# Kernel tuning notes

Hardware: AMD Instinct MI355X
Metric: run time of the kernel (lower is better)

Reference implementation:

```python
import jax, jax.numpy as jnp
import numpy as np

N_HEADS = 16
ROPE_DIMS = 16
SEQ_LEN = 512


def _rope_cache(T, dtype=jnp.float32):
    rd = ROPE_DIMS
    freqs = 1.0 / (10000.0 ** (jnp.arange(0, rd, 2, dtype=jnp.float32) / rd))  # [rd/2]
    t = jnp.arange(T, dtype=jnp.float32)
    ang = jnp.outer(t, freqs)  # [T, rd/2]
    return jnp.cos(ang).astype(dtype), jnp.sin(ang).astype(dtype)


def _apply_rope(x, cos, sin):
    # x: [B, H, T, hd]; partial RoPE on first ROPE_DIMS dims
    rd = ROPE_DIMS
    x_rope, x_pass = x[..., :rd], x[..., rd:]
    x1, x2 = x_rope[..., : rd // 2], x_rope[..., rd // 2 :]
    # cos/sin: [T, rd/2] -> broadcast over B, H
    out = jnp.concatenate([x1 * cos - x2 * sin, x2 * cos + x1 * sin], axis=-1)
    return jnp.concatenate([out, x_pass], axis=-1)


def setup_inputs() -> dict:
    key = jax.random.key(0)
    k1, k2, k3 = jax.random.split(key, 3)
    B, T, C = 8, SEQ_LEN, 2048
    x = jax.random.normal(k1, (B, T, C), dtype=jnp.float32)
    Wqkv = jax.random.normal(k2, (3 * C, C), dtype=jnp.float32) * (1.0 / np.sqrt(C))
    Wout = jax.random.normal(k3, (C, C), dtype=jnp.float32) * (1.0 / np.sqrt(C))
    return {"x": x, "Wqkv": Wqkv, "Wout": Wout}


def reference(x, Wqkv, Wout):
    B, T, C = x.shape
    H = N_HEADS
    hd = C // H
    # fused QKV projection
    qkv = jnp.einsum("btc,fc->btf", x, Wqkv)  # [B, T, 3C]
    qkv = qkv.reshape(B, T, 3, H, hd)
    q, k, v = qkv[:, :, 0], qkv[:, :, 1], qkv[:, :, 2]  # [B, T, H, hd]
    q = jnp.transpose(q, (0, 2, 1, 3))  # [B, H, T, hd]
    k = jnp.transpose(k, (0, 2, 1, 3))
    v = jnp.transpose(v, (0, 2, 1, 3))
    cos, sin = _rope_cache(T, dtype=x.dtype)
    q = _apply_rope(q, cos, sin)
    k = _apply_rope(k, cos, sin)
    # causal SDPA
    scale = 1.0 / np.sqrt(hd)
    scores = jnp.einsum("bhqd,bhkd->bhqk", q, k) * scale
    causal = jnp.tril(jnp.ones((T, T), dtype=bool))
    scores = jnp.where(causal, scores, jnp.finfo(scores.dtype).min)
    attn = jax.nn.softmax(scores, axis=-1)
    y = jnp.einsum("bhqk,bhkd->bhqd", attn, v)  # [B, H, T, hd]
    y = jnp.transpose(y, (0, 2, 1, 3)).reshape(B, T, C)
    return jnp.einsum("btc,oc->bto", y, Wout)
```

## Files before the change

### kernel.cpp

```cpp
#include <hip/hip_runtime.h>

typedef __bf16 bf16_t;
typedef __bf16 bf16x4 __attribute__((ext_vector_type(4)));
typedef __bf16 bf16x8 __attribute__((ext_vector_type(8)));
typedef float f32x4 __attribute__((ext_vector_type(4)));

#define GLB(p) ((const __attribute__((address_space(1))) void*)(p))
#define LDS(p) ((__attribute__((address_space(3))) void*)(p))

__global__ void f32_to_bf16(const float* __restrict__ src, bf16_t* __restrict__ dst, int n8)
{
    const int i = blockIdx.x * 256 + threadIdx.x;
    if (i >= n8) return;
    const f32x4 a = *(const f32x4*)&src[(size_t)i * 8];
    const f32x4 b = *(const f32x4*)&src[(size_t)i * 8 + 4];
    bf16x8 h = {(bf16_t)a[0], (bf16_t)a[1], (bf16_t)a[2], (bf16_t)a[3],
                (bf16_t)b[0], (bf16_t)b[1], (bf16_t)b[2], (bf16_t)b[3]};
    *(bf16x8*)&dst[(size_t)i * 8] = h;
}

#define LDB4(d, kk, S)                                                         \
    { _Pragma("unroll") for (int nt = 0; nt < 4; ++nt)                         \
        bfr[S][nt] = *(const bf16x8*)&smem[sBe + (d) * 32768 + (kk) * 8192 + nt * 512]; }

#define LDA4(d, kk, g, S)                                                      \
    { _Pragma("unroll") for (int i = 0; i < 4; ++i)                            \
        afr[S][i] = *(const bf16x8*)&smem[sAe + (d) * 32768 + (kk) * 8192 + ((g) * 4 + i) * 512]; }

#define MM4(g, SA, SB)                                                         \
    { _Pragma("unroll") for (int i = 0; i < 4; ++i)                            \
        _Pragma("unroll") for (int nt = 0; nt < 4; ++nt)                       \
            acc[(g) * 4 + i][nt] = __builtin_amdgcn_mfma_f32_16x16x32_bf16(    \
                afr[SA][i], bfr[SB][nt], acc[(g) * 4 + i][nt], 0, 0, 0); }

#define PHASE_TAIL(g, SA, SB)                                                  \
    __builtin_amdgcn_s_barrier();                                              \
    asm volatile("s_waitcnt lgkmcnt(0)" ::: "memory");                         \
    __builtin_amdgcn_s_setprio(1);                                             \
    MM4(g, SA, SB);                                                            \
    __builtin_amdgcn_s_setprio(0);                                             \
    __builtin_amdgcn_s_barrier();

template <int MODE>
__global__ __launch_bounds__(512, 2)
void gemm256(const bf16_t* __restrict__ A, const bf16_t* __restrict__ Bm, int K,
             bf16_t* __restrict__ o0, bf16_t* __restrict__ o1, bf16_t* __restrict__ o2,
             float* __restrict__ of)
{
    __shared__ __align__(16) bf16_t smem[65536];

    const int tid  = threadIdx.x;
    const int lane = tid & 63;
    const int w    = tid >> 6;
    const int wr   = w >> 2;
    const int wc   = w & 3;
    const int quad = lane >> 4;
    const int qcol = lane & 15;
    const int m0   = blockIdx.x * 256;
    const int n0   = blockIdx.y * 256;

    f32x4 acc[8][4];
#pragma unroll
    for (int i = 0; i < 8; ++i)
#pragma unroll
        for (int j = 0; j < 4; ++j)
            acc[i][j] = (f32x4){0.f, 0.f, 0.f, 0.f};

    const int srow = w * 16 + (lane >> 2);
    const int scg  = (lane & 3) ^ ((lane >> 3) & 3);
    const bf16_t* Ag = A  + (size_t)(m0 + srow) * K + scg * 8;
    const bf16_t* Bg = Bm + (size_t)(n0 + srow) * K + scg * 8;

    auto STAGE = [&](int d, int t, int hh) {
        const int isA = hh & 1;
        const int kh  = hh >> 1;
        const bf16_t* g = (isA ? Ag : Bg) + t * 64 + kh * 32;
        bf16_t* l = &smem[d * 32768 + kh * 8192 + (isA ? 0 : 16384) + w * 512];
        __builtin_amdgcn_global_load_lds(GLB(g), LDS(l), 16, 0, 0);
        __builtin_amdgcn_global_load_lds(GLB(g + (size_t)128 * K), LDS(l + 4096), 16, 0, 0);
    };

    const int rs8 = (quad ^ ((qcol >> 1) & 3)) * 8;
    const int sAe = (wr * 128 + qcol) * 32 + rs8;
    const int sBe = 16384 + (wc * 64 + qcol) * 32 + rs8;

    bf16x8 afr[2][4], bfr[2][4];

    const int NT  = K >> 6;
    const int NIT = NT >> 1;

    STAGE(0, 0, 0); STAGE(0, 0, 1); STAGE(0, 0, 2); STAGE(0, 0, 3);
    STAGE(1, 1, 0); STAGE(1, 1, 1); STAGE(1, 1, 2);
    asm volatile("s_waitcnt vmcnt(6)" ::: "memory");
    __builtin_amdgcn_s_barrier();

    for (int J = 0; J < NIT - 1; ++J) {
        const int t = 2 * J;
        LDB4(0, 0, 0); LDA4(0, 0, 0, 0); STAGE(1, t + 1, 3);
        PHASE_TAIL(0, 0, 0);
        LDA4(0, 0, 1, 1); STAGE(0, t + 2, 0);
        PHASE_TAIL(1, 1, 0);
        LDB4(0, 1, 1); LDA4(0, 1, 0, 0); STAGE(0, t + 2, 1);
        PHASE_TAIL(0, 0, 1);
        LDA4(0, 1, 1, 1); STAGE(0, t + 2, 2);
        asm volatile("s_waitcnt vmcnt(6)" ::: "memory");
        PHASE_TAIL(1, 1, 1);
        LDB4(1, 0, 0); LDA4(1, 0, 0, 0); STAGE(0, t + 2, 3);
        PHASE_TAIL(0, 0, 0);
        LDA4(1, 0, 1, 1); STAGE(1, t + 3, 0);
        PHASE_TAIL(1, 1, 0);
        LDB4(1, 1, 1); LDA4(1, 1, 0, 0); STAGE(1, t + 3, 1);
        PHASE_TAIL(0, 0, 1);
        LDA4(1, 1, 1, 1); STAGE(1, t + 3, 2);
        asm volatile("s_waitcnt vmcnt(6)" ::: "memory");
        PHASE_TAIL(1, 1, 1);
    }

    {
        const int t = NT - 2;
        LDB4(0, 0, 0); LDA4(0, 0, 0, 0); STAGE(1, t + 1, 3);
        PHASE_TAIL(0, 0, 0);
        LDA4(0, 0, 1, 1);
        PHASE_TAIL(1, 1, 0);
        LDB4(0, 1, 1); LDA4(0, 1, 0, 0);
        PHASE_TAIL(0, 0, 1);
        LDA4(0, 1, 1, 1);
        asm volatile("s_waitcnt vmcnt(0)" ::: "memory");
        PHASE_TAIL(1, 1, 1);
        LDB4(1, 0, 0); LDA4(1, 0, 0, 0);
        PHASE_TAIL(0, 0, 0);
        LDA4(1, 0, 1, 1);
        PHASE_TAIL(1, 1, 0);
        LDB4(1, 1, 1); LDA4(1, 1, 0, 0);
        PHASE_TAIL(0, 0, 1);
        LDA4(1, 1, 1, 1);
        __builtin_amdgcn_s_barrier();
        asm volatile("s_waitcnt lgkmcnt(0)" ::: "memory");
        __builtin_amdgcn_s_setprio(1);
        MM4(1, 1, 1);
        __builtin_amdgcn_s_setprio(0);
    }

#pragma unroll
    for (int mt = 0; mt < 8; ++mt) {
#pragma unroll
        for (int nt = 0; nt < 4; ++nt) {
#pragma unroll
            for (int r = 0; r < 4; ++r) {
                const int m = m0 + wr * 128 + mt * 16 + quad * 4 + r;
                const int f = n0 + wc * 64 + nt * 16 + qcol;
                const float val = acc[mt][nt][r];
                if (MODE == 0) {
                    const int b     = m >> 9;
                    const int t     = m & 511;
                    const int which = f >> 11;
                    const int h     = (f >> 7) & 15;
                    const int d     = f & 127;
                    if (which == 2) {
                        o2[((size_t)(((b << 4) + h) * 128 + d) << 9) + t] = (bf16_t)val;
                    } else {
                        bf16_t* dst = (which == 0) ? o0 : o1;
                        dst[(size_t)(((b << 4) + h) * 512 + t) * 128 + d] = (bf16_t)val;
                    }
                } else {
                    of[(size_t)m * 2048 + f] = val;
                }
            }
        }
    }
}

template <int MODE>
__global__ __launch_bounds__(256)
void gemm_bt(const bf16_t* __restrict__ A, const bf16_t* __restrict__ Bm, int K,
             bf16_t* __restrict__ o0, bf16_t* __restrict__ o1, bf16_t* __restrict__ o2,
             float* __restrict__ of)
{
    __shared__ __align__(16) bf16_t As[128 * 32];
    __shared__ __align__(16) bf16_t Bs[128 * 32];
    const int tid  = threadIdx.x;
    const int lane = tid & 63;
    const int w    = tid >> 6;
    const int wm   = (w & 1) * 64;
    const int wn   = (w >> 1) * 64;
    const int m0   = blockIdx.x * 128;
    const int n0   = blockIdx.y * 128;
    const int quad = lane >> 4;
    const int qcol = lane & 15;

    f32x4 acc[4][4];
#pragma unroll
    for (int i = 0; i < 4; ++i)
#pragma unroll
        for (int j = 0; j < 4; ++j)
            acc[i][j] = (f32x4){0.f, 0.f, 0.f, 0.f};

    const int rc = lane >> 2;
    const int cg = (lane & 3) ^ (rc & 3);
    const int c0 = 2 * w, c1 = 2 * w + 1;
    const bf16_t* ag0 = A  + (size_t)(m0 + 16 * c0 + rc) * K + cg * 8;
    const bf16_t* ag1 = A  + (size_t)(m0 + 16 * c1 + rc) * K + cg * 8;
    const bf16_t* bg0 = Bm + (size_t)(n0 + 16 * c0 + rc) * K + cg * 8;
    const bf16_t* bg1 = Bm + (size_t)(n0 + 16 * c1 + rc) * K + cg * 8;
    bf16_t* al0 = &As[c0 * 512];
    bf16_t* al1 = &As[c1 * 512];
    bf16_t* bl0 = &Bs[c0 * 512];
    bf16_t* bl1 = &Bs[c1 * 512];

    const int swz8 = (quad ^ (qcol & 3)) * 8;

    for (int k0 = 0; k0 < K; k0 += 32) {
        __syncthreads();
        __builtin_amdgcn_global_load_lds(GLB(ag0 + k0), LDS(al0), 16, 0, 0);
        __builtin_amdgcn_global_load_lds(GLB(ag1 + k0), LDS(al1), 16, 0, 0);
        __builtin_amdgcn_global_load_lds(GLB(bg0 + k0), LDS(bl0), 16, 0, 0);
        __builtin_amdgcn_global_load_lds(GLB(bg1 + k0), LDS(bl1), 16, 0, 0);
        __syncthreads();

        bf16x8 af[4], bf[4];
#pragma unroll
        for (int mt = 0; mt < 4; ++mt)
            af[mt] = *(const bf16x8*)&As[(wm + mt * 16 + qcol) * 32 + swz8];
#pragma unroll
        for (int nt = 0; nt < 4; ++nt)
            bf[nt] = *(const bf16x8*)&Bs[(wn + nt * 16 + qcol) * 32 + swz8];
#pragma unroll
        for (int mt = 0; mt < 4; ++mt)
#pragma unroll
            for (int nt = 0; nt < 4; ++nt)
                acc[mt][nt] = __builtin_amdgcn_mfma_f32_16x16x32_bf16(af[mt], bf[nt], acc[mt][nt], 0, 0, 0);
    }

#pragma unroll
    for (int mt = 0; mt < 4; ++mt) {
#pragma unroll
        for (int nt = 0; nt < 4; ++nt) {
#pragma unroll
            for (int r = 0; r < 4; ++r) {
                const int m = m0 + wm + mt * 16 + quad * 4 + r;
                const int f = n0 + wn + nt * 16 + qcol;
                const float val = acc[mt][nt][r];
                of[(size_t)m * 2048 + f] = val;
            }
        }
    }
}

__global__ void rope_kernel(bf16_t* __restrict__ q, bf16_t* __restrict__ k)
{
    const int id  = blockIdx.x * 256 + threadIdx.x;
    const int arr = id >> 19;
    const int rem = id & ((1 << 19) - 1);
    const int bh  = rem >> 12;
    const int t   = (rem >> 3) & 511;
    const int d   = rem & 7;

    bf16_t* p = (arr ? k : q) + (size_t)(bh * 512 + t) * 128;
    const float x1 = (float)p[d];
    const float x2 = (float)p[d + 8];
    const float freq = __expf(-(float)d * 1.1512925464970229f);
    const float ang  = (float)t * freq;
    const float c = cosf(ang), s = sinf(ang);
    p[d]     = (bf16_t)(x1 * c - x2 * s);
    p[d + 8] = (bf16_t)(x2 * c + x1 * s);
}

#define PLD 72

__global__ __launch_bounds__(256)
void flash_attn(const bf16_t* __restrict__ q, const bf16_t* __restrict__ k,
                const bf16_t* __restrict__ vT, bf16_t* __restrict__ y)
{
    const int bid = blockIdx.x;
    const int sg  = bid >> 7;
    const int qtb = (sg < 2) ? sg : 5 - sg;
    const int rem = bid & 127;
    const int h   = rem & 15;
    const int b   = rem >> 4;
    const int tid  = threadIdx.x;
    const int lane = tid & 63;
    const int w    = tid >> 6;
    const int quad = lane >> 4;
    const int qcol = lane & 15;

    __shared__ __align__(16) bf16_t Ps[128 * PLD];

    const bf16_t* qb  = q  + (size_t)((b * 16 + h) * 512) * 128;
    const bf16_t* kb  = k  + (size_t)((b * 16 + h) * 512) * 128;
    const bf16_t* vtb = vT + (size_t)((b * 16 + h) * 128) * 512;

    bf16x8 qfrag[2][4];
#pragma unroll
    for (int qg = 0; qg < 2; ++qg) {
        const int qrow = qtb * 128 + w * 32 + qg * 16 + qcol;
#pragma unroll
        for (int kc = 0; kc < 4; ++kc)
            qfrag[qg][kc] = *(const bf16x8*)&qb[(size_t)qrow * 128 + kc * 32 + quad * 8];
    }

    f32x4 acc_o[2][8];
#pragma unroll
    for (int qg = 0; qg < 2; ++qg)
#pragma unroll
        for (int nt = 0; nt < 8; ++nt) acc_o[qg][nt] = (f32x4){0.f, 0.f, 0.f, 0.f};
    float m_run[2] = {-INFINITY, -INFINITY};
    float l_run[2] = {0.f, 0.f};
    const float scale = 0.08838834764831845f;

    const int wq_min  = qtb * 128 + w * 32;
    const int kt_last = 2 * qtb + 1;
    for (int kt = 0; kt <= kt_last; ++kt) {
        if (kt * 64 > wq_min + 31) break;
        const bool need_mask = ((kt + 1) * 64 > wq_min);

        f32x4 sacc[2][4];
#pragma unroll
        for (int qg = 0; qg < 2; ++qg)
#pragma unroll
            for (int mt = 0; mt < 4; ++mt) sacc[qg][mt] = (f32x4){0.f, 0.f, 0.f, 0.f};
#pragma unroll
        for (int mt = 0; mt < 4; ++mt)
#pragma unroll
            for (int kc = 0; kc < 4; ++kc) {
                bf16x8 af = *(const bf16x8*)&kb[(size_t)(kt * 64 + mt * 16 + qcol) * 128 + kc * 32 + quad * 8];
                sacc[0][mt] = __builtin_amdgcn_mfma_f32_16x16x32_bf16(af, qfrag[0][kc], sacc[0][mt], 0, 0, 0);
                sacc[1][mt] = __builtin_amdgcn_mfma_f32_16x16x32_bf16(af, qfrag[1][kc], sacc[1][mt], 0, 0, 0);
            }

#pragma unroll
        for (int qg = 0; qg < 2; ++qg) {
            float s[16];
#pragma unroll
            for (int mt = 0; mt < 4; ++mt)
#pragma unroll
                for (int r = 0; r < 4; ++r)
                    s[mt * 4 + r] = sacc[qg][mt][r] * scale;
            if (need_mask) {
                const int qglob = qtb * 128 + w * 32 + qg * 16 + qcol;
#pragma unroll
                for (int mt = 0; mt < 4; ++mt)
#pragma unroll
                    for (int r = 0; r < 4; ++r)
                        if (kt * 64 + mt * 16 + quad * 4 + r > qglob)
                            s[mt * 4 + r] = -1e30f;
            }

            float mx = s[0];
#pragma unroll
            for (int i = 1; i < 16; ++i) mx = fmaxf(mx, s[i]);
            mx = fmaxf(mx, __shfl_xor(mx, 16));
            mx = fmaxf(mx, __shfl_xor(mx, 32));
            const float m_new = fmaxf(m_run[qg], mx);
            const float alpha = __expf(m_run[qg] - m_new);
            float p16[16];
            float sum = 0.f;
#pragma unroll
            for (int i = 0; i < 16; ++i) { p16[i] = __expf(s[i] - m_new); sum += p16[i]; }
            sum += __shfl_xor(sum, 16);
            sum += __shfl_xor(sum, 32);
            l_run[qg] = l_run[qg] * alpha + sum;
            m_run[qg] = m_new;

#pragma unroll
            for (int mt = 0; mt < 4; ++mt) {
                bf16x4 pb = {(bf16_t)p16[mt * 4 + 0], (bf16_t)p16[mt * 4 + 1],
                             (bf16_t)p16[mt * 4 + 2], (bf16_t)p16[mt * 4 + 3]};
                *(bf16x4*)&Ps[(w * 32 + qg * 16 + qcol) * PLD + mt * 16 + quad * 4] = pb;
            }

#pragma unroll
            for (int r = 0; r < 4; ++r) {
                const float ar = __shfl(alpha, quad * 4 + r);
#pragma unroll
                for (int nt = 0; nt < 8; ++nt)
                    acc_o[qg][nt][r] *= ar;
            }
        }

#pragma unroll
        for (int kc2 = 0; kc2 < 2; ++kc2) {
            bf16x8 pf0 = *(const bf16x8*)&Ps[(w * 32 + qcol) * PLD + kc2 * 32 + quad * 8];
            bf16x8 pf1 = *(const bf16x8*)&Ps[(w * 32 + 16 + qcol) * PLD + kc2 * 32 + quad * 8];
#pragma unroll
            for (int nt = 0; nt < 8; ++nt) {
                bf16x8 vf = *(const bf16x8*)&vtb[(size_t)(nt * 16 + qcol) * 512 + kt * 64 + kc2 * 32 + quad * 8];
                acc_o[0][nt] = __builtin_amdgcn_mfma_f32_16x16x32_bf16(pf0, vf, acc_o[0][nt], 0, 0, 0);
                acc_o[1][nt] = __builtin_amdgcn_mfma_f32_16x16x32_bf16(pf1, vf, acc_o[1][nt], 0, 0, 0);
            }
        }
    }

#pragma unroll
    for (int qg = 0; qg < 2; ++qg) {
#pragma unroll
        for (int r = 0; r < 4; ++r) {
            const float lr = __shfl(l_run[qg], quad * 4 + r);
            const int t  = qtb * 128 + w * 32 + qg * 16 + quad * 4 + r;
#pragma unroll
            for (int nt = 0; nt < 8; ++nt) {
                const int cc = h * 128 + nt * 16 + qcol;
                y[(size_t)(b * 512 + t) * 2048 + cc] = (bf16_t)(acc_o[qg][nt][r] / lr);
            }
        }
    }
}

extern "C" void kernel_launch(void* const* d_in, const int* in_sizes, int n_in,
                              void* d_out, int out_size, void* d_ws, size_t ws_size,
                              hipStream_t stream)
{
    (void)in_sizes; (void)n_in; (void)out_size; (void)ws_size;

    const float* x    = (const float*)d_in[0];
    const float* Wqkv = (const float*)d_in[1];
    const float* Wout = (const float*)d_in[2];
    float* out = (float*)d_out;

    const size_t SEG = (size_t)8 * 16 * 512 * 128;
    bf16_t* q      = (bf16_t*)d_ws;
    bf16_t* k      = q + SEG;
    bf16_t* vT     = k + SEG;
    bf16_t* xb     = vT + SEG;
    bf16_t* y      = xb;
    bf16_t* Wqkvb  = xb + SEG;
    bf16_t* Woutb  = Wqkvb + (size_t)6144 * 2048;

    f32_to_bf16<<<(8388608 / 8) / 256, 256, 0, stream>>>(x, xb, 8388608 / 8);
    f32_to_bf16<<<(12582912 / 8) / 256, 256, 0, stream>>>(Wqkv, Wqkvb, 12582912 / 8);
    f32_to_bf16<<<(4194304 / 8) / 256, 256, 0, stream>>>(Wout, Woutb, 4194304 / 8);
    gemm256<0><<<dim3(4096 / 256, 6144 / 256), 512, 0, stream>>>(xb, Wqkvb, 2048, q, k, vT, nullptr);
    rope_kernel<<<(2 * 128 * 512 * 8) / 256, 256, 0, stream>>>(q, k);
    flash_attn<<<512, 256, 0, stream>>>(q, k, vT, y);
    gemm_bt<1><<<dim3(4096 / 128, 2048 / 128), 256, 0, stream>>>(y, Woutb, 2048, nullptr, nullptr, nullptr, out);
}
```

Before: 381.3 us.

## Stage K and V^T tiles in shared memory for flash attention

Each K and V^T tile is now loaded cooperatively into padded LDS buffers once per block, instead of every wave reading its fragments directly from global memory. This is meant to cut redundant global and L2 traffic, since all four waves share the same K/V tile. The score MFMA loop is also moved inside the per-qg loop to lower register pressure. In exchange it adds two barriers per key tile and LDS usage that may reduce occupancy. Waves past the causal boundary must keep looping to join the barriers, which adds idle iterations.

Result: no change. 377.7 us (-0.9%).

```diff
diff --git a/kernel.cpp b/kernel.cpp
--- a/kernel.cpp
+++ b/kernel.cpp
@@ -265,6 +265,8 @@
     p[d + 8] = (bf16_t)(x2 * c + x1 * s);
 }
 
+#define KLD 132
+#define VLD 68
 #define PLD 72
 
 __global__ __launch_bounds__(256)
@@ -283,6 +285,8 @@
     const int quad = lane >> 4;
     const int qcol = lane & 15;
 
+    __shared__ __align__(16) bf16_t Ks[64 * KLD];
+    __shared__ __align__(16) bf16_t VTs[128 * VLD];
     __shared__ __align__(16) bf16_t Ps[128 * PLD];
 
     const bf16_t* qb  = q  + (size_t)((b * 16 + h) * 512) * 128;
@@ -310,31 +314,41 @@
     const int wq_min  = qtb * 128 + w * 32;
     const int kt_last = 2 * qtb + 1;
     for (int kt = 0; kt <= kt_last; ++kt) {
-        if (kt * 64 > wq_min + 31) break;
+        __syncthreads();
+#pragma unroll
+        for (int p = 0; p < 4; ++p) {
+            const int r = p * 16 + (tid >> 4), c = (tid & 15) * 8;
+            *(uint4*)&Ks[r * KLD + c] = *(const uint4*)&kb[(size_t)(kt * 64 + r) * 128 + c];
+        }
+#pragma unroll
+        for (int p = 0; p < 4; ++p) {
+            const int r = p * 32 + (tid >> 3), c = (tid & 7) * 8;
+            *(uint4*)&VTs[r * VLD + c] = *(const uint4*)&vtb[(size_t)r * 512 + kt * 64 + c];
+        }
+        __syncthreads();
+
+        if (kt * 64 > wq_min + 31) continue;
         const bool need_mask = ((kt + 1) * 64 > wq_min);
 
-        f32x4 sacc[2][4];
-#pragma unroll
-        for (int qg = 0; qg < 2; ++qg)
-#pragma unroll
-            for (int mt = 0; mt < 4; ++mt) sacc[qg][mt] = (f32x4){0.f, 0.f, 0.f, 0.f};
-#pragma unroll
-        for (int mt = 0; mt < 4; ++mt)
-#pragma unroll
-            for (int kc = 0; kc < 4; ++kc) {
-                bf16x8 af = *(const bf16x8*)&kb[(size_t)(kt * 64 + mt * 16 + qcol) * 128 + kc * 32 + quad * 8];
-                sacc[0][mt] = __builtin_amdgcn_mfma_f32_16x16x32_bf16(af, qfrag[0][kc], sacc[0][mt], 0, 0, 0);
-                sacc[1][mt] = __builtin_amdgcn_mfma_f32_16x16x32_bf16(af, qfrag[1][kc], sacc[1][mt], 0, 0, 0);
-            }
-
 #pragma unroll
         for (int qg = 0; qg < 2; ++qg) {
+            f32x4 sacc[4];
+#pragma unroll
+            for (int mt = 0; mt < 4; ++mt) sacc[mt] = (f32x4){0.f, 0.f, 0.f, 0.f};
+#pragma unroll
+            for (int mt = 0; mt < 4; ++mt)
+#pragma unroll
+                for (int kc = 0; kc < 4; ++kc) {
+                    bf16x8 af = *(const bf16x8*)&Ks[(mt * 16 + qcol) * KLD + kc * 32 + quad * 8];
+                    sacc[mt] = __builtin_amdgcn_mfma_f32_16x16x32_bf16(af, qfrag[qg][kc], sacc[mt], 0, 0, 0);
+                }
+
             float s[16];
 #pragma unroll
             for (int mt = 0; mt < 4; ++mt)
 #pragma unroll
                 for (int r = 0; r < 4; ++r)
-                    s[mt * 4 + r] = sacc[qg][mt][r] * scale;
+                    s[mt * 4 + r] = sacc[mt][r] * scale;
             if (need_mask) {
                 const int qglob = qtb * 128 + w * 32 + qg * 16 + qcol;
 #pragma unroll
@@ -383,7 +397,7 @@
             bf16x8 pf1 = *(const bf16x8*)&Ps[(w * 32 + 16 + qcol) * PLD + kc2 * 32 + quad * 8];
 #pragma unroll
             for (int nt = 0; nt < 8; ++nt) {
-                bf16x8 vf = *(const bf16x8*)&vtb[(size_t)(nt * 16 + qcol) * 512 + kt * 64 + kc2 * 32 + quad * 8];
+                bf16x8 vf = *(const bf16x8*)&VTs[(nt * 16 + qcol) * VLD + kc2 * 32 + quad * 8];
                 acc_o[0][nt] = __builtin_amdgcn_mfma_f32_16x16x32_bf16(pf0, vf, acc_o[0][nt], 0, 0, 0);
                 acc_o[1][nt] = __builtin_amdgcn_mfma_f32_16x16x32_bf16(pf1, vf, acc_o[1][nt], 0, 0, 0);
             }
```
